# Kernel tuning notes

Measured on AMD Instinct MI355X. Metric: run time of the kernel, lower is better.

Reference implementation:

```python
import jax, jax.numpy as jnp
import numpy as np

H = 8      # num_heads
DH = 80    # head_dim = embed_dim // num_heads


def setup_inputs() -> dict:
    key = jax.random.key(0)
    ks = jax.random.split(key, 7)
    B, T, S = 8, 4096, 77
    hidden, embed, ctx = 640, 640, 768
    sc_h = 1.0 / np.sqrt(hidden)
    sc_c = 1.0 / np.sqrt(ctx)
    sc_e = 1.0 / np.sqrt(embed)
    return {
        "tokens": jax.random.normal(ks[0], (B, T, hidden), jnp.float32),
        "context": jax.random.normal(ks[1], (B, S, ctx), jnp.float32),
        "Wq": jax.random.normal(ks[2], (hidden, embed), jnp.float32) * sc_h,
        "Wk": jax.random.normal(ks[3], (ctx, embed), jnp.float32) * sc_c,
        "Wv": jax.random.normal(ks[4], (ctx, embed), jnp.float32) * sc_c,
        "Wo": jax.random.normal(ks[5], (embed, hidden), jnp.float32) * sc_e,
        "bo": jnp.zeros((hidden,), jnp.float32),
    }


def reference(tokens, context, Wq, Wk, Wv, Wo, bo):
    B, T, _ = tokens.shape
    S = context.shape[1]
    Q = (tokens @ Wq).reshape(B, T, H, DH)    # B T H D
    K = (context @ Wk).reshape(B, S, H, DH)   # B S H D
    V = (context @ Wv).reshape(B, S, H, DH)
    scores = jnp.einsum('bthd,bshd->bhts', Q, K) / jnp.sqrt(jnp.float32(DH))
    attn = jax.nn.softmax(scores, axis=-1)    # B H T S
    ctx_vecs = jnp.einsum('bhts,bshd->bthd', attn, V).reshape(B, T, H * DH)
    return ctx_vecs @ Wo + bo
```

## Files before the change

kernel.cpp:

```cpp
#include <hip/hip_runtime.h>
#include <hip/hip_bf16.h>
#include <hip/hip_fp16.h>

typedef __attribute__((ext_vector_type(4))) float f32x4;
typedef __attribute__((ext_vector_type(8))) _Float16 f16x8;
typedef __attribute__((ext_vector_type(8))) unsigned short u16x8;

__device__ __forceinline__ unsigned short f2h(float f) {
    _Float16 h = (_Float16)f;
    return __builtin_bit_cast(unsigned short, h);
}

#define GLOAD_LDS16(gp, lp) __builtin_amdgcn_global_load_lds( \
    (const __attribute__((address_space(1))) void*)(gp), \
    (__attribute__((address_space(3))) void*)(lp), 16, 0, 0)
#define PRIO1() __builtin_amdgcn_s_setprio(1)
#define PRIO0() __builtin_amdgcn_s_setprio(0)

__global__ void cvt_kernel(const float* __restrict__ in, ushort* __restrict__ out, int n4) {
    int stride = gridDim.x * blockDim.x;
    for (int i = blockIdx.x * blockDim.x + threadIdx.x; i < n4; i += stride) {
        float4 v = ((const float4*)in)[i];
        ushort4 o;
        o.x = f2h(v.x); o.y = f2h(v.y); o.z = f2h(v.z); o.w = f2h(v.w);
        ((ushort4*)out)[i] = o;
    }
}

__global__ void transpose_cvt2(const float* __restrict__ Wk, const float* __restrict__ Wv,
                               ushort* __restrict__ WkvT) {
    __shared__ float tile[32][33];
    const int z = blockIdx.z;
    const float* src = z ? Wv : Wk;
    ushort* dst = WkvT + (size_t)z * 640 * 768;
    const int R = 768, C = 640;
    int tx = threadIdx.x, ty = threadIdx.y;
    int c = blockIdx.x * 32 + tx;
    int r0 = blockIdx.y * 32;
#pragma unroll
    for (int i = ty; i < 32; i += 8) {
        int r = r0 + i;
        tile[i][tx] = (r < R && c < C) ? src[(size_t)r * C + c] : 0.f;
    }
    __syncthreads();
    int rr = r0 + tx;
    int c0 = blockIdx.x * 32;
#pragma unroll
    for (int i = ty; i < 32; i += 8) {
        int cc = c0 + i;
        if (cc < C && rr < R) dst[(size_t)cc * R + rr] = f2h(tile[tx][i]);
    }
}

__global__ void pack_wfrag(const float* __restrict__ W, ushort* __restrict__ WF) {
    int g = blockIdx.x * 256 + threadIdx.x;
    if (g >= 51200) return;
    int lane = g & 63;
    int fi = (g >> 6) % 10;
    int kt = ((g >> 6) / 10) % 10;
    int h  = (g >> 6) / 100;
    int ni = fi >> 1, kk = fi & 1;
    int n  = h * 80 + ni * 16 + (lane & 15);
    int k0 = kt * 64 + kk * 32 + (lane >> 4) * 8;
    u16x8 o;
#pragma unroll
    for (int e = 0; e < 8; ++e) o[e] = f2h(W[(size_t)(k0 + e) * 640 + n]);
    *(u16x8*)&WF[(size_t)g * 8] = o;
}

__global__ void pack_kvfrag(const ushort* __restrict__ KVb,
                            ushort* __restrict__ KF, ushort* __restrict__ VF) {
    int g = blockIdx.x * 256 + threadIdx.x;
    if (g >= 61440) return;
    int lane = g & 63;
    int fi = (g >> 6) % 15;
    int bh = (g >> 6) / 15;
    int b = bh >> 3, h = bh & 7;
    int ni = fi / 3, kk = fi % 3;
    int l15 = lane & 15, lhi = lane >> 4;
    int sr = ni * 16 + l15; if (sr > 76) sr = 76;
    int d0 = kk * 32 + lhi * 8;
    u16x8 ko, vo;
#pragma unroll
    for (int e = 0; e < 8; ++e)
        ko[e] = KVb[((size_t)b * 77 + sr) * 1280 + h * 80 + d0 + e];
    int dv = ni * 16 + l15;
    int s0 = kk * 32 + lhi * 8;
#pragma unroll
    for (int e = 0; e < 8; ++e) {
        int s = s0 + e;
        vo[e] = (s < 77) ? KVb[((size_t)b * 77 + s) * 1280 + 640 + h * 80 + dv] : (ushort)0;
    }
    *(u16x8*)&KF[(size_t)g * 8] = ko;
    *(u16x8*)&VF[(size_t)g * 8] = vo;
}

template<int OUT_F16, int HAS_BIAS>
__global__ __launch_bounds__(256) void gemm_bt(
    const ushort* __restrict__ A, const ushort* __restrict__ Bt,
    void* __restrict__ C, const float* __restrict__ bias,
    int M, int N, int K)
{
    __shared__ ushort As[128 * 64];
    __shared__ ushort Bs[128 * 64];
    const int tid = threadIdx.x;
    const int lane = tid & 63;
    const int w = tid >> 6;
    const int wr = (w >> 1) * 64, wc = (w & 1) * 64;
    const int m0 = blockIdx.x * 128, n0 = blockIdx.y * 128;
    const int l15 = lane & 15, lhi = lane >> 4;

    f32x4 acc[4][4] = {};

    for (int k0 = 0; k0 < K; k0 += 64) {
        __syncthreads();
#pragma unroll
        for (int i = 0; i < 4; ++i) {
            int c = i * 256 + tid;
            int m = m0 + (c >> 3);
            if (m > M - 1) m = M - 1;
            GLOAD_LDS16(A + (size_t)m * K + k0 + (c & 7) * 8, &As[c * 8]);
        }
#pragma unroll
        for (int i = 0; i < 4; ++i) {
            int c = i * 256 + tid;
            GLOAD_LDS16(Bt + (size_t)(n0 + (c >> 3)) * K + k0 + (c & 7) * 8, &Bs[c * 8]);
        }
        __syncthreads();
#pragma unroll
        for (int kk = 0; kk < 2; ++kk) {
            f16x8 af[4], bfr[4];
#pragma unroll
            for (int mi = 0; mi < 4; ++mi)
                af[mi] = *(const f16x8*)&As[(wr + mi * 16 + l15) * 64 + kk * 32 + lhi * 8];
#pragma unroll
            for (int ni = 0; ni < 4; ++ni)
                bfr[ni] = *(const f16x8*)&Bs[(wc + ni * 16 + l15) * 64 + kk * 32 + lhi * 8];
#pragma unroll
            for (int mi = 0; mi < 4; ++mi)
#pragma unroll
                for (int ni = 0; ni < 4; ++ni)
                    acc[mi][ni] = __builtin_amdgcn_mfma_f32_16x16x32_f16(
                        af[mi], bfr[ni], acc[mi][ni], 0, 0, 0);
        }
    }

#pragma unroll
    for (int mi = 0; mi < 4; ++mi)
#pragma unroll
        for (int ni = 0; ni < 4; ++ni)
#pragma unroll
            for (int r = 0; r < 4; ++r) {
                int row = m0 + wr + mi * 16 + lhi * 4 + r;
                int col = n0 + wc + ni * 16 + l15;
                if (row < M) {
                    float v = acc[mi][ni][r];
                    if (HAS_BIAS) v += bias[col];
                    if (OUT_F16) ((ushort*)C)[(size_t)row * N + col] = f2h(v);
                    else         ((float*)C)[(size_t)row * N + col] = v;
                }
            }
}

__global__ __launch_bounds__(512, 2) void fused_attn(
    const float* __restrict__ tokens, const ushort* __restrict__ WqF,
    const ushort* __restrict__ KF, const ushort* __restrict__ VF,
    const ushort* __restrict__ WoF, const float* __restrict__ bo,
    float* __restrict__ out)
{
    __shared__ __align__(16) ushort lds[40960];
    const int tid = threadIdx.x;
    const int lane = tid & 63;
    const int w = tid >> 6;
    const int l15 = lane & 15, lhi = lane >> 4;
    const int tt = blockIdx.x, b = blockIdx.y;
    const size_t rowbase = (size_t)b * 4096 + (size_t)tt * 64;

    const int srow = tid >> 3;
    const int sc8  = tid & 7;
    const int sphys = sc8 ^ (srow & 7);

    const ushort* WqFb = WqF + (size_t)w * 10 * 5120;
    const ushort* WoFb = WoF + (size_t)w * 10 * 5120;
    const ushort* KFb  = KF + (size_t)(b * 8 + w) * 15 * 512;
    const ushort* VFb  = VF + (size_t)(b * 8 + w) * 15 * 512;

    {
        const float4* sp = (const float4*)(tokens + (rowbase + srow) * 640 + sc8 * 8);
        float4 v0 = sp[0], v1 = sp[1];
        u16x8 o;
        o[0]=f2h(v0.x); o[1]=f2h(v0.y); o[2]=f2h(v0.z); o[3]=f2h(v0.w);
        o[4]=f2h(v1.x); o[5]=f2h(v1.y); o[6]=f2h(v1.z); o[7]=f2h(v1.w);
        *(u16x8*)&lds[srow * 64 + sphys * 8] = o;
    }
    f16x8 BbE[10], BbO[10];
#pragma unroll
    for (int f = 0; f < 10; ++f)
        BbE[f] = *(const f16x8*)(WqFb + f * 512 + lane * 8);
    __syncthreads();

    f32x4 qacc[4][5] = {};
#define QSTEP(BCUR, BNXT, KT, CURB, NXTB) do { \
    float4 s0_, s1_; \
    const int kt_ = (KT); \
    if (kt_ < 9) { \
        const float4* sp_ = (const float4*)(tokens + (rowbase + srow) * 640 + (kt_+1)*64 + sc8*8); \
        s0_ = sp_[0]; s1_ = sp_[1]; \
        _Pragma("unroll") for (int f = 0; f < 10; ++f) \
            (BNXT)[f] = *(const f16x8*)(WqFb + (size_t)(kt_+1)*5120 + f*512 + lane*8); \
    } \
    _Pragma("unroll") for (int kk = 0; kk < 2; ++kk) { \
        f16x8 af[4]; \
        _Pragma("unroll") for (int mi = 0; mi < 4; ++mi) { \
            int row_ = mi*16 + l15; \
            af[mi] = *(const f16x8*)&lds[(CURB) + row_*64 + (((kk*4 + lhi) ^ (row_ & 7)))*8]; \
        } \
        PRIO1(); \
        _Pragma("unroll") for (int mi = 0; mi < 4; ++mi) \
        _Pragma("unroll") for (int ni = 0; ni < 5; ++ni) \
            qacc[mi][ni] = __builtin_amdgcn_mfma_f32_16x16x32_f16(af[mi], (BCUR)[ni*2+kk], qacc[mi][ni], 0, 0, 0); \
        PRIO0(); \
    } \
    if (kt_ < 9) { \
        u16x8 o_; \
        o_[0]=f2h(s0_.x); o_[1]=f2h(s0_.y); o_[2]=f2h(s0_.z); o_[3]=f2h(s0_.w); \
        o_[4]=f2h(s1_.x); o_[5]=f2h(s1_.y); o_[6]=f2h(s1_.z); o_[7]=f2h(s1_.w); \
        *(u16x8*)&lds[(NXTB) + srow*64 + sphys*8] = o_; \
    } \
    __syncthreads(); \
} while (0)

    for (int kp = 0; kp < 5; ++kp) {
        QSTEP(BbE, BbO, 2*kp,     0,    4096);
        QSTEP(BbO, BbE, 2*kp + 1, 4096, 0);
    }
#undef QSTEP

    const int qoff = w * 5120;
#pragma unroll
    for (int mi = 0; mi < 4; ++mi)
#pragma unroll
        for (int ni = 0; ni < 5; ++ni)
#pragma unroll
            for (int r = 0; r < 4; ++r)
                lds[qoff + (mi*16 + lhi*4 + r)*80 + ni*16 + l15] = f2h(qacc[mi][ni][r]);
    __builtin_amdgcn_sched_barrier(0);

    const f16x8 zf = {};
    f32x4 sa[4][5] = {};
    {
        f16x8 bk[15];
#pragma unroll
        for (int f = 0; f < 15; ++f)
            bk[f] = *(const f16x8*)(KFb + f * 512 + lane * 8);
#pragma unroll
        for (int kk = 0; kk < 3; ++kk) {
            f16x8 aq[4];
            const int kcol = (kk < 2) ? (kk*32 + lhi*8) : (64 + (lhi & 1)*8);
#pragma unroll
            for (int mi = 0; mi < 4; ++mi) {
                aq[mi] = *(const f16x8*)&lds[qoff + (mi*16 + l15)*80 + kcol];
                if (kk == 2 && lhi >= 2) aq[mi] = zf;
            }
            PRIO1();
#pragma unroll
            for (int mi = 0; mi < 4; ++mi)
#pragma unroll
                for (int ni = 0; ni < 5; ++ni)
                    sa[mi][ni] = __builtin_amdgcn_mfma_f32_16x16x32_f16(aq[mi], bk[ni*3+kk], sa[mi][ni], 0, 0, 0);
            PRIO0();
        }
    }
    __builtin_amdgcn_sched_barrier(0);

    const float sc = 0.11180339887498949f;
#pragma unroll
    for (int mi = 0; mi < 4; ++mi)
#pragma unroll
        for (int r = 0; r < 4; ++r) {
            float v0 = sa[mi][0][r]*sc, v1 = sa[mi][1][r]*sc, v2 = sa[mi][2][r]*sc,
                  v3 = sa[mi][3][r]*sc, v4 = sa[mi][4][r]*sc;
            bool ok4 = l15 < 13;
            float mx = fmaxf(fmaxf(v0, v1), fmaxf(v2, v3));
            if (ok4) mx = fmaxf(mx, v4);
#pragma unroll
            for (int off = 1; off < 16; off <<= 1) mx = fmaxf(mx, __shfl_xor(mx, off, 16));
            float p0 = __expf(v0-mx), p1 = __expf(v1-mx), p2 = __expf(v2-mx), p3 = __expf(v3-mx);
            float p4 = ok4 ? __expf(v4-mx) : 0.f;
            float sm = p0+p1+p2+p3+p4;
#pragma unroll
            for (int off = 1; off < 16; off <<= 1) sm += __shfl_xor(sm, off, 16);
            float inv = 1.f / sm;
            int row = mi*16 + lhi*4 + r;
            lds[qoff + row*80 + 0*16 + l15] = f2h(p0*inv);
            lds[qoff + row*80 + 1*16 + l15] = f2h(p1*inv);
            lds[qoff + row*80 + 2*16 + l15] = f2h(p2*inv);
            lds[qoff + row*80 + 3*16 + l15] = f2h(p3*inv);
            lds[qoff + row*80 + 4*16 + l15] = f2h(p4*inv);
        }
    __builtin_amdgcn_sched_barrier(0);

    f32x4 oa[4][5] = {};
    {
        f16x8 bv[15];
#pragma unroll
        for (int f = 0; f < 15; ++f)
            bv[f] = *(const f16x8*)(VFb + f * 512 + lane * 8);
#pragma unroll
        for (int kk = 0; kk < 3; ++kk) {
            f16x8 ap[4];
            const int kcol = (kk < 2) ? (kk*32 + lhi*8) : (64 + (lhi & 1)*8);
#pragma unroll
            for (int mi = 0; mi < 4; ++mi) {
                ap[mi] = *(const f16x8*)&lds[qoff + (mi*16 + l15)*80 + kcol];
                if (kk == 2 && lhi >= 2) ap[mi] = zf;
            }
            PRIO1();
#pragma unroll
            for (int mi = 0; mi < 4; ++mi)
#pragma unroll
                for (int ni = 0; ni < 5; ++ni)
                    oa[mi][ni] = __builtin_amdgcn_mfma_f32_16x16x32_f16(ap[mi], bv[ni*3+kk], oa[mi][ni], 0, 0, 0);
            PRIO0();
        }
    }
    __syncthreads();

#pragma unroll
    for (int mi = 0; mi < 4; ++mi)
#pragma unroll
        for (int ni = 0; ni < 5; ++ni)
#pragma unroll
            for (int r = 0; r < 4; ++r) {
                int row = mi*16 + lhi*4 + r;
                int col = w*80 + ni*16 + l15;
                int slot = col >> 3;
                int phys = (((slot & ~7) | ((slot ^ row) & 7)) << 3) | (col & 7);
                lds[row*640 + phys] = f2h(oa[mi][ni][r]);
            }
    __syncthreads();

    f32x4 cacc[4][5] = {};
#pragma unroll
    for (int f = 0; f < 10; ++f)
        BbE[f] = *(const f16x8*)(WoFb + f * 512 + lane * 8);
#define OSTEP(BCUR, BNXT, KT) do { \
    const int kt_ = (KT); \
    if (kt_ < 9) { \
        _Pragma("unroll") for (int f = 0; f < 10; ++f) \
            (BNXT)[f] = *(const f16x8*)(WoFb + (size_t)(kt_+1)*5120 + f*512 + lane*8); \
    } \
    _Pragma("unroll") for (int kk = 0; kk < 2; ++kk) { \
        f16x8 af[4]; \
        _Pragma("unroll") for (int mi = 0; mi < 4; ++mi) { \
            int row_ = mi*16 + l15; \
            af[mi] = *(const f16x8*)&lds[row_*640 + ((kt_*8 + ((kk*4 + lhi) ^ (row_ & 7))))*8]; \
        } \
        PRIO1(); \
        _Pragma("unroll") for (int mi = 0; mi < 4; ++mi) \
        _Pragma("unroll") for (int ni = 0; ni < 5; ++ni) \
            cacc[mi][ni] = __builtin_amdgcn_mfma_f32_16x16x32_f16(af[mi], (BCUR)[ni*2+kk], cacc[mi][ni], 0, 0, 0); \
        PRIO0(); \
    } \
} while (0)
    for (int kp = 0; kp < 5; ++kp) {
        OSTEP(BbE, BbO, 2*kp);
        OSTEP(BbO, BbE, 2*kp + 1);
    }
#undef OSTEP

#pragma unroll
    for (int ni = 0; ni < 5; ++ni) {
        int col = w*80 + ni*16 + l15;
        float bvl = bo[col];
#pragma unroll
        for (int mi = 0; mi < 4; ++mi)
#pragma unroll
            for (int r = 0; r < 4; ++r)
                out[(rowbase + mi*16 + lhi*4 + r) * 640 + col] = cacc[mi][ni][r] + bvl;
    }
}

extern "C" void kernel_launch(void* const* d_in, const int* in_sizes, int n_in,
                              void* d_out, int out_size, void* d_ws, size_t ws_size,
                              hipStream_t stream) {
    (void)in_sizes; (void)n_in; (void)out_size; (void)ws_size;
    const float* tokens  = (const float*)d_in[0];
    const float* context = (const float*)d_in[1];
    const float* Wq = (const float*)d_in[2];
    const float* Wk = (const float*)d_in[3];
    const float* Wv = (const float*)d_in[4];
    const float* Wo = (const float*)d_in[5];
    const float* bo = (const float*)d_in[6];
    float* out = (float*)d_out;

    ushort* ws   = (ushort*)d_ws;
    ushort* ctx16 = ws;
    ushort* WkvT = ctx16 + (size_t)616 * 768;
    ushort* KVb  = WkvT + (size_t)1280 * 768;
    ushort* WqF  = KVb  + (size_t)616 * 1280;
    ushort* WoF  = WqF  + (size_t)640 * 640;
    ushort* KF   = WoF  + (size_t)640 * 640;
    ushort* VF   = KF   + (size_t)61440 * 8;

    cvt_kernel<<<462, 256, 0, stream>>>(context, ctx16, 616 * 768 / 4);
    transpose_cvt2<<<dim3(20, 24, 2), dim3(32, 8), 0, stream>>>(Wk, Wv, WkvT);
    pack_wfrag<<<200, 256, 0, stream>>>(Wq, WqF);
    pack_wfrag<<<200, 256, 0, stream>>>(Wo, WoF);
    gemm_bt<1, 0><<<dim3(5, 10), 256, 0, stream>>>(ctx16, WkvT, KVb, nullptr, 616, 1280, 768);
    pack_kvfrag<<<240, 256, 0, stream>>>(KVb, KF, VF);
    fused_attn<<<dim3(64, 8), 512, 0, stream>>>(tokens, WqF, KF, VF, WoF, bo, out);
}
```

Baseline: 117.4 us.

## Stage full token tile in LDS upfront and drop per-step barriers in Q projection

The fp16-converted 64x640 token tile is now loaded into LDS once before the Q projection, using a 4-deep register prefetch ring. The old scheme double-buffered 64-column slices and needed a __syncthreads after each of the 10 k-steps. This removes nine block barriers and the interleaved global-load/convert work from the MFMA loop. In exchange, the prologue is longer and exposes the token load latency before any math starts, and more registers are held during the prologue.

Result: slower. 123.6 us (+5.3%).

```diff
diff --git a/kernel.cpp b/kernel.cpp
--- a/kernel.cpp
+++ b/kernel.cpp
@@ -176,22 +176,33 @@
     const int tt = blockIdx.x, b = blockIdx.y;
     const size_t rowbase = (size_t)b * 4096 + (size_t)tt * 64;
 
-    const int srow = tid >> 3;
-    const int sc8  = tid & 7;
-    const int sphys = sc8 ^ (srow & 7);
-
     const ushort* WqFb = WqF + (size_t)w * 10 * 5120;
     const ushort* WoFb = WoF + (size_t)w * 10 * 5120;
     const ushort* KFb  = KF + (size_t)(b * 8 + w) * 15 * 512;
     const ushort* VFb  = VF + (size_t)(b * 8 + w) * 15 * 512;
 
+    const int srow = tid >> 3;
+    const int sc8  = tid & 7;
     {
-        const float4* sp = (const float4*)(tokens + (rowbase + srow) * 640 + sc8 * 8);
-        float4 v0 = sp[0], v1 = sp[1];
-        u16x8 o;
-        o[0]=f2h(v0.x); o[1]=f2h(v0.y); o[2]=f2h(v0.z); o[3]=f2h(v0.w);
-        o[4]=f2h(v1.x); o[5]=f2h(v1.y); o[6]=f2h(v1.z); o[7]=f2h(v1.w);
-        *(u16x8*)&lds[srow * 64 + sphys * 8] = o;
+        const float* tbase = tokens + (rowbase + srow) * 640 + sc8 * 8;
+        float4 sA[4], sB[4];
+#pragma unroll
+        for (int kt = 0; kt < 4; ++kt) {
+            sA[kt] = ((const float4*)(tbase + kt * 64))[0];
+            sB[kt] = ((const float4*)(tbase + kt * 64))[1];
+        }
+#pragma unroll
+        for (int kt = 0; kt < 10; ++kt) {
+            const int sl = kt & 3;
+            u16x8 o;
+            o[0]=f2h(sA[sl].x); o[1]=f2h(sA[sl].y); o[2]=f2h(sA[sl].z); o[3]=f2h(sA[sl].w);
+            o[4]=f2h(sB[sl].x); o[5]=f2h(sB[sl].y); o[6]=f2h(sB[sl].z); o[7]=f2h(sB[sl].w);
+            *(u16x8*)&lds[srow * 640 + (kt * 8 + (sc8 ^ (srow & 7))) * 8] = o;
+            if (kt + 4 < 10) {
+                sA[sl] = ((const float4*)(tbase + (kt + 4) * 64))[0];
+                sB[sl] = ((const float4*)(tbase + (kt + 4) * 64))[1];
+            }
+        }
     }
     f16x8 BbE[10], BbO[10];
 #pragma unroll
@@ -200,12 +211,9 @@
     __syncthreads();
 
     f32x4 qacc[4][5] = {};
-#define QSTEP(BCUR, BNXT, KT, CURB, NXTB) do { \
-    float4 s0_, s1_; \
+#define QSTEP(BCUR, BNXT, KT) do { \
     const int kt_ = (KT); \
     if (kt_ < 9) { \
-        const float4* sp_ = (const float4*)(tokens + (rowbase + srow) * 640 + (kt_+1)*64 + sc8*8); \
-        s0_ = sp_[0]; s1_ = sp_[1]; \
         _Pragma("unroll") for (int f = 0; f < 10; ++f) \
             (BNXT)[f] = *(const f16x8*)(WqFb + (size_t)(kt_+1)*5120 + f*512 + lane*8); \
     } \
@@ -213,7 +221,7 @@
         f16x8 af[4]; \
         _Pragma("unroll") for (int mi = 0; mi < 4; ++mi) { \
             int row_ = mi*16 + l15; \
-            af[mi] = *(const f16x8*)&lds[(CURB) + row_*64 + (((kk*4 + lhi) ^ (row_ & 7)))*8]; \
+            af[mi] = *(const f16x8*)&lds[row_*640 + (kt_*8 + ((kk*4 + lhi) ^ (row_ & 7)))*8]; \
         } \
         PRIO1(); \
         _Pragma("unroll") for (int mi = 0; mi < 4; ++mi) \
@@ -221,20 +229,13 @@
             qacc[mi][ni] = __builtin_amdgcn_mfma_f32_16x16x32_f16(af[mi], (BCUR)[ni*2+kk], qacc[mi][ni], 0, 0, 0); \
         PRIO0(); \
     } \
-    if (kt_ < 9) { \
-        u16x8 o_; \
-        o_[0]=f2h(s0_.x); o_[1]=f2h(s0_.y); o_[2]=f2h(s0_.z); o_[3]=f2h(s0_.w); \
-        o_[4]=f2h(s1_.x); o_[5]=f2h(s1_.y); o_[6]=f2h(s1_.z); o_[7]=f2h(s1_.w); \
-        *(u16x8*)&lds[(NXTB) + srow*64 + sphys*8] = o_; \
-    } \
-    __syncthreads(); \
 } while (0)
-
     for (int kp = 0; kp < 5; ++kp) {
-        QSTEP(BbE, BbO, 2*kp,     0,    4096);
-        QSTEP(BbO, BbE, 2*kp + 1, 4096, 0);
+        QSTEP(BbE, BbO, 2*kp);
+        QSTEP(BbO, BbE, 2*kp + 1);
     }
 #undef QSTEP
+    __syncthreads();
 
     const int qoff = w * 5120;
 #pragma unroll
@@ -354,7 +355,7 @@
         f16x8 af[4]; \
         _Pragma("unroll") for (int mi = 0; mi < 4; ++mi) { \
             int row_ = mi*16 + l15; \
-            af[mi] = *(const f16x8*)&lds[row_*640 + ((kt_*8 + ((kk*4 + lhi) ^ (row_ & 7))))*8]; \
+            af[mi] = *(const f16x8*)&lds[row_*640 + (kt_*8 + ((kk*4 + lhi) ^ (row_ & 7)))*8]; \
         } \
         PRIO1(); \
         _Pragma("unroll") for (int mi = 0; mi < 4; ++mi) \
```
